# Kernel tuning notes

Hardware: AMD Instinct MI355X
Metric: run time of the kernel (lower is better)

Reference implementation:

```python
import jax, jax.numpy as jnp
import numpy as np

N = 1024      # n_nodes
S = 32        # state_dim
M = 32        # message_dim
STEPS = 5     # n_steps


def setup_inputs() -> dict:
    key = jax.random.key(0)
    ks = jax.random.split(key, 12)
    w = lambda k, shape: jax.random.normal(k, shape, jnp.float32) * 0.02
    return {
        "J": jax.random.normal(ks[0], (N, N), jnp.float32),
        "b": jax.random.normal(ks[1], (N,), jnp.float32),
        # message_passing MLP (Linear(2S+3->M), Linear(M->M), Linear(M->M))
        "W1": w(ks[2], (M, 2 * S + 3)), "b1": jnp.zeros((M,), jnp.float32),
        "W2": w(ks[3], (M, M)),         "b2": jnp.zeros((M,), jnp.float32),
        "W3": w(ks[4], (M, M)),         "b3": jnp.zeros((M,), jnp.float32),
        # GRU(input=S+M, hidden=S). h0 is always zero in the original forward,
        # so weight_hh never contributes (only bias_hh does) and is omitted.
        "W_ih": w(ks[5], (3 * S, S + M)),
        "b_ih": w(ks[6], (3 * S,)),
        "b_hh": w(ks[7], (3 * S,)),
        # readout MLP (Linear(S->M), Linear(M->M), Linear(M->2))
        "R1": w(ks[8], (M, S)),  "rb1": jnp.zeros((M,), jnp.float32),
        "R2": w(ks[9], (M, M)),  "rb2": jnp.zeros((M,), jnp.float32),
        "R3": w(ks[10], (2, M)), "rb3": jnp.zeros((2,), jnp.float32),
    }


def reference(J, b, W1, b1, W2, b2, W3, b3, W_ih, b_ih, b_hh, R1, rb1, R2, rb2, R3, rb3):
    # Split first linear over the concat [h_i, h_j, J_ij, b_i, b_j] so the
    # [N, N, 2S+3] concat tensor is never materialized.
    W1a, W1b = W1[:, :S], W1[:, S:2 * S]
    wJ, wbi, wbj = W1[:, 2 * S], W1[:, 2 * S + 1], W1[:, 2 * S + 2]

    def step(h, _):
        hi = h @ W1a.T                       # [N, M] (sender part)
        hj = h @ W1b.T                       # [N, M] (receiver part)
        pre = (hi[:, None, :] + hj[None, :, :]
               + J[:, :, None] * wJ
               + b[:, None, None] * wbi
               + b[None, :, None] * wbj
               + b1)                          # [N, N, M]
        x = jax.nn.relu(pre)
        x = jax.nn.relu(x @ W2.T + b2)
        x = jax.nn.relu(x @ W3.T + b3)       # message_i_j: [N, N, M]
        m = x.sum(0)                          # message to node j: sum over senders i
        # GRU with zero initial hidden state: h' = (1-z) * n_gate
        gi = jnp.concatenate([h, m], axis=-1) @ W_ih.T + b_ih  # [N, 3S]
        r = jax.nn.sigmoid(gi[:, :S] + b_hh[:S])
        z = jax.nn.sigmoid(gi[:, S:2 * S] + b_hh[S:2 * S])
        n = jnp.tanh(gi[:, 2 * S:] + r * b_hh[2 * S:])
        return (1.0 - z) * n, None

    h0 = jnp.zeros((N, S), J.dtype)
    h, _ = jax.lax.scan(step, h0, None, length=STEPS)

    r = jax.nn.relu(h @ R1.T + rb1)
    r = jax.nn.relu(r @ R2.T + rb2)
    r = jax.nn.relu(r @ R3.T + rb3)          # [N, 2]
    return jax.nn.sigmoid(r)
```

## Files before the change

kernel.cpp:

```cpp
#include <hip/hip_runtime.h>
#include <math.h>

#define NN 1024

typedef __attribute__((ext_vector_type(8))) short bf16x8;
typedef __attribute__((ext_vector_type(4))) float f32x4;
typedef __attribute__((ext_vector_type(4))) unsigned int u32x4;

__device__ __forceinline__ float sigmoidf_(float x) { return 1.0f / (1.0f + __expf(-x)); }

__device__ __forceinline__ unsigned int pk_bf16(float a, float b) {
    unsigned int ua = __float_as_uint(a), ub = __float_as_uint(b);
    ua += 0x7fffu + ((ua >> 16) & 1u);
    ub += 0x7fffu + ((ub >> 16) & 1u);
    return (ua >> 16) | (ub & 0xffff0000u);
}
__device__ __forceinline__ unsigned short f2bf_rne(float a) {
    unsigned int ua = __float_as_uint(a);
    ua += 0x7fffu + ((ua >> 16) & 1u);
    return (unsigned short)(ua >> 16);
}

struct Ctx {
    bf16x8 w2a0, w2a1, w3a0, w3a1;
    f32x4 b2v0, b2v1, b3v0, b3v1;
    float wj8[8];
};

__device__ __forceinline__ void make_ctx(Ctx& c, int p, int q,
    const float* __restrict__ W1, const float* __restrict__ W2,
    const float* __restrict__ b2, const float* __restrict__ W3,
    const float* __restrict__ b3)
{
    union FU { bf16x8 v; unsigned short s[8]; } t0, t1, t2, t3;
#pragma unroll
    for (int jj = 0; jj < 8; jj++) {
        int k = q * 8 + jj;
        t0.s[jj] = f2bf_rne(W2[p * 32 + k]);
        t1.s[jj] = f2bf_rne(W2[(16 + p) * 32 + k]);
        t2.s[jj] = f2bf_rne(W3[p * 32 + k]);
        t3.s[jj] = f2bf_rne(W3[(16 + p) * 32 + k]);
        c.wj8[jj] = W1[k * 67 + 64];
    }
    c.w2a0 = t0.v; c.w2a1 = t1.v; c.w3a0 = t2.v; c.w3a1 = t3.v;
#pragma unroll
    for (int r = 0; r < 4; r++) {
        c.b2v0[r] = b2[q * 4 + r];  c.b2v1[r] = b2[16 + q * 4 + r];
        c.b3v0[r] = b3[q * 4 + r];  c.b3v1[r] = b3[16 + q * 4 + r];
    }
}

__device__ __forceinline__ void gru_row(int s, float hval, float mval, float bj,
    const float* __restrict__ Wih, const float* __restrict__ bih,
    const float* __restrict__ bhh, const float* __restrict__ W1,
    const float* __restrict__ b1, float& hn, float& uacc, float& vacc)
{
    float g0 = bih[s], g1 = bih[32 + s], g2 = bih[64 + s];
#pragma unroll 8
    for (int k = 0; k < 32; k++) {
        float hk = __shfl(hval, k, 32);
        float mk = __shfl(mval, k, 32);
        g0 = fmaf(Wih[s * 64 + k],             hk, g0);
        g0 = fmaf(Wih[s * 64 + 32 + k],        mk, g0);
        g1 = fmaf(Wih[(32 + s) * 64 + k],      hk, g1);
        g1 = fmaf(Wih[(32 + s) * 64 + 32 + k], mk, g1);
        g2 = fmaf(Wih[(64 + s) * 64 + k],      hk, g2);
        g2 = fmaf(Wih[(64 + s) * 64 + 32 + k], mk, g2);
    }
    float r = sigmoidf_(g0 + bhh[s]);
    float z = sigmoidf_(g1 + bhh[32 + s]);
    float n = tanhf(g2 + r * bhh[64 + s]);
    hn = (1.0f - z) * n;
    float ua = bj * W1[s * 67 + 65];
    float va = fmaf(bj, W1[s * 67 + 66], b1[s]);
#pragma unroll 8
    for (int k = 0; k < 32; k++) {
        float hk = __shfl(hn, k, 32);
        ua = fmaf(W1[s * 67 + k],      hk, ua);
        va = fmaf(W1[s * 67 + 32 + k], hk, va);
    }
    uacc = ua; vacc = va;
}

__device__ __forceinline__ void readout_row(int s, int j, float hn,
    const float* __restrict__ R1, const float* __restrict__ rb1,
    const float* __restrict__ R2, const float* __restrict__ rb2,
    const float* __restrict__ R3, const float* __restrict__ rb3,
    float* __restrict__ out)
{
    float a1 = rb1[s];
#pragma unroll 8
    for (int k = 0; k < 32; k++) a1 = fmaf(R1[s * 32 + k], __shfl(hn, k, 32), a1);
    a1 = fmaxf(a1, 0.f);
    float a2 = rb2[s];
#pragma unroll 8
    for (int k = 0; k < 32; k++) a2 = fmaf(R2[s * 32 + k], __shfl(a1, k, 32), a2);
    a2 = fmaxf(a2, 0.f);
    float a3 = (s < 2) ? rb3[s] : 0.f;
#pragma unroll 8
    for (int k = 0; k < 32; k++) {
        float a2k = __shfl(a2, k, 32);
        if (s < 2) a3 = fmaf(R3[s * 32 + k], a2k, a3);
    }
    if (s < 2) out[j * 2 + s] = sigmoidf_(fmaxf(a3, 0.f));
}

__global__ __launch_bounds__(256) void k_pre(
    const float* __restrict__ J, const float* __restrict__ b,
    const float* __restrict__ W1, const float* __restrict__ b1,
    float* __restrict__ Jt, float* __restrict__ h,
    float* __restrict__ u0, float* __restrict__ v)
{
    __shared__ float tile[32][33];
    const int t = blockIdx.x;
    const int tid = threadIdx.x;
    if (t < 1024) {
        int tx = (t & 31) * 32, ty = (t >> 5) * 32;
        int x = tid & 31, y = tid >> 5;
#pragma unroll
        for (int r = 0; r < 4; r++)
            tile[y + 8 * r][x] = J[(size_t)(ty + y + 8 * r) * NN + tx + x];
        __syncthreads();
#pragma unroll
        for (int r = 0; r < 4; r++)
            Jt[(size_t)(tx + y + 8 * r) * NN + ty + x] = tile[x][y + 8 * r];
    } else {
        int idx = (t - 1024) * 256 + tid;
        int row = idx >> 5, mm = idx & 31;
        float bi = b[row];
        h[idx]  = 0.f;
        u0[idx] = bi * W1[mm * 67 + 65];
        v[idx]  = fmaf(bi, W1[mm * 67 + 66], b1[mm]);
    }
}

__global__ __launch_bounds__(256, 4) void k_step(
    const float* __restrict__ Jt, const float* __restrict__ W1,
    const float* __restrict__ W2, const float* __restrict__ b2,
    const float* __restrict__ W3, const float* __restrict__ b3,
    const float* __restrict__ Wih, const float* __restrict__ bih,
    const float* __restrict__ bhh, const float* __restrict__ b,
    const float* __restrict__ b1,
    const float* __restrict__ R1, const float* __restrict__ rb1,
    const float* __restrict__ R2, const float* __restrict__ rb2,
    const float* __restrict__ R3, const float* __restrict__ rb3,
    float* __restrict__ h, float* __restrict__ v,
    const float* __restrict__ ui, float* __restrict__ uo,
    float* __restrict__ out, int do_out)
{
    __shared__ float red[4 * 32];

    const int tid = threadIdx.x;
    const int w = tid >> 6;
    const int l = tid & 63;
    const int p = l & 15;
    const int q = l >> 4;
    const int j = blockIdx.x;

    Ctx c; make_ctx(c, p, q, W1, W2, b2, W3, b3);
    const float* Jtrow = Jt + (size_t)j * NN;

    float vv[8];
#pragma unroll
    for (int jj = 0; jj < 8; jj++) vv[jj] = v[j * 32 + q * 8 + jj];

    const int s0 = (p | ((l & 16) << 1)) << 2;
    const int s1 = s0 + 64;
    const bool qlo = (l & 32) == 0;

    f32x4 acc0 = {0.f, 0.f, 0.f, 0.f}, acc1 = {0.f, 0.f, 0.f, 0.f};

    int i0 = w * 256 + p;
    float  jw = Jtrow[i0];
    float4 ua = *(const float4*)(ui + i0 * 32 + q * 8);
    float4 ub = *(const float4*)(ui + i0 * 32 + q * 8 + 4);

#pragma unroll 2
    for (int t = 0; t < 16; ++t) {
        const float  jw_c = jw;
        const float4 ua_c = ua;
        const float4 ub_c = ub;
        if (t < 15) {
            const int in = w * 256 + (t + 1) * 16 + p;
            jw = Jtrow[in];
            ua = *(const float4*)(ui + in * 32 + q * 8);
            ub = *(const float4*)(ui + in * 32 + q * 8 + 4);
        }

        float xr[8];
        xr[0] = fmaxf(fmaf(jw_c, c.wj8[0], ua_c.x + vv[0]), 0.f);
        xr[1] = fmaxf(fmaf(jw_c, c.wj8[1], ua_c.y + vv[1]), 0.f);
        xr[2] = fmaxf(fmaf(jw_c, c.wj8[2], ua_c.z + vv[2]), 0.f);
        xr[3] = fmaxf(fmaf(jw_c, c.wj8[3], ua_c.w + vv[3]), 0.f);
        xr[4] = fmaxf(fmaf(jw_c, c.wj8[4], ub_c.x + vv[4]), 0.f);
        xr[5] = fmaxf(fmaf(jw_c, c.wj8[5], ub_c.y + vv[5]), 0.f);
        xr[6] = fmaxf(fmaf(jw_c, c.wj8[6], ub_c.z + vv[6]), 0.f);
        xr[7] = fmaxf(fmaf(jw_c, c.wj8[7], ub_c.w + vv[7]), 0.f);

        union BU { u32x4 u4; bf16x8 v; unsigned int d[4]; } bx;
#pragma unroll
        for (int cc = 0; cc < 4; cc++) bx.d[cc] = pk_bf16(xr[2 * cc], xr[2 * cc + 1]);

        f32x4 c0 = __builtin_amdgcn_mfma_f32_16x16x32_bf16(c.w2a0, bx.v, c.b2v0, 0, 0, 0);
        f32x4 c1 = __builtin_amdgcn_mfma_f32_16x16x32_bf16(c.w2a1, bx.v, c.b2v1, 0, 0, 0);

        const int d0 = (int)pk_bf16(fmaxf(c0[0], 0.f), fmaxf(c0[1], 0.f));
        const int d1 = (int)pk_bf16(fmaxf(c0[2], 0.f), fmaxf(c0[3], 0.f));
        const int d2 = (int)pk_bf16(fmaxf(c1[0], 0.f), fmaxf(c1[1], 0.f));
        const int d3 = (int)pk_bf16(fmaxf(c1[2], 0.f), fmaxf(c1[3], 0.f));

        const int A0 = __builtin_amdgcn_ds_bpermute(s0, d0);
        const int A1 = __builtin_amdgcn_ds_bpermute(s0, d1);
        const int A2 = __builtin_amdgcn_ds_bpermute(s1, d0);
        const int A3 = __builtin_amdgcn_ds_bpermute(s1, d1);
        const int B0 = __builtin_amdgcn_ds_bpermute(s0, d2);
        const int B1 = __builtin_amdgcn_ds_bpermute(s0, d3);
        const int B2 = __builtin_amdgcn_ds_bpermute(s1, d2);
        const int B3 = __builtin_amdgcn_ds_bpermute(s1, d3);

        union BU yr;
        yr.d[0] = (unsigned)(qlo ? A0 : B0);
        yr.d[1] = (unsigned)(qlo ? A1 : B1);
        yr.d[2] = (unsigned)(qlo ? A2 : B2);
        yr.d[3] = (unsigned)(qlo ? A3 : B3);

        f32x4 e0 = __builtin_amdgcn_mfma_f32_16x16x32_bf16(c.w3a0, yr.v, c.b3v0, 0, 0, 0);
        f32x4 e1 = __builtin_amdgcn_mfma_f32_16x16x32_bf16(c.w3a1, yr.v, c.b3v1, 0, 0, 0);
#pragma unroll
        for (int r = 0; r < 4; r++) {
            acc0[r] += fmaxf(e0[r], 0.f);
            acc1[r] += fmaxf(e1[r], 0.f);
        }
    }

#pragma unroll
    for (int bit = 1; bit < 16; bit <<= 1) {
#pragma unroll
        for (int r = 0; r < 4; r++) {
            acc0[r] += __shfl_xor(acc0[r], bit);
            acc1[r] += __shfl_xor(acc1[r], bit);
        }
    }
    if (p == 0) {
#pragma unroll
        for (int r = 0; r < 4; r++) {
            red[w * 32 + q * 4 + r]      = acc0[r];
            red[w * 32 + 16 + q * 4 + r] = acc1[r];
        }
    }
    __syncthreads();

    if (tid < 32) {
        const int s = tid;
        float mval = red[s] + red[32 + s] + red[64 + s] + red[96 + s];
        float hn, uacc, vacc;
        gru_row(s, h[j * 32 + s], mval, b[j], Wih, bih, bhh, W1, b1, hn, uacc, vacc);
        h[j * 32 + s] = hn;
        v[j * 32 + s] = vacc;
        uo[j * 32 + s] = uacc;
        if (do_out) readout_row(s, j, hn, R1, rb1, R2, rb2, R3, rb3, out);
    }
}

extern "C" void kernel_launch(void* const* d_in, const int* in_sizes, int n_in,
                              void* d_out, int out_size, void* d_ws, size_t ws_size,
                              hipStream_t stream)
{
    const float* J   = (const float*)d_in[0];
    const float* b   = (const float*)d_in[1];
    const float* W1  = (const float*)d_in[2];
    const float* b1  = (const float*)d_in[3];
    const float* W2  = (const float*)d_in[4];
    const float* b2  = (const float*)d_in[5];
    const float* W3  = (const float*)d_in[6];
    const float* b3  = (const float*)d_in[7];
    const float* Wih = (const float*)d_in[8];
    const float* bih = (const float*)d_in[9];
    const float* bhh = (const float*)d_in[10];
    const float* R1  = (const float*)d_in[11];
    const float* rb1 = (const float*)d_in[12];
    const float* R2  = (const float*)d_in[13];
    const float* rb2 = (const float*)d_in[14];
    const float* R3  = (const float*)d_in[15];
    const float* rb3 = (const float*)d_in[16];

    float* out = (float*)d_out;
    float* ws  = (float*)d_ws;
    float* h  = ws;
    float* v  = ws + 32768;
    float* u0 = ws + 65536;
    float* u1 = ws + 98304;
    float* Jt = ws + 131072;

    k_pre<<<1152, 256, 0, stream>>>(J, b, W1, b1, Jt, h, u0, v);
    for (int s = 0; s < 5; s++) {
        const float* ui = (s & 1) ? u1 : u0;
        float*       uo = (s & 1) ? u0 : u1;
        k_step<<<1024, 256, 0, stream>>>(Jt, W1, W2, b2, W3, b3, Wih, bih,
                                         bhh, b, b1, R1, rb1, R2, rb2, R3,
                                         rb3, h, v, ui, uo, out,
                                         (s == 4) ? 1 : 0);
    }
}
```

Measured before the change: 223.2 us.

## Parallelize GRU and readout tail across threads and deepen operand prefetch

Replaces the 32-lane shuffle-based GRU, message-projection and readout with shared-memory staged dot products spread over up to 192 threads using vectorized weight loads. The main loop now prefetches two iterations ahead with alternating register sets. The first step launches a doubled grid whose extra blocks redo the message loop and then exit. This adds wasted work and extra barriers in exchange for a shorter serial tail.

Measured after the change: 241.4 us. +8.1%, slower.

```diff
diff --git a/kernel.cpp b/kernel.cpp
--- a/kernel.cpp
+++ b/kernel.cpp
@@ -48,61 +48,6 @@
         c.b2v0[r] = b2[q * 4 + r];  c.b2v1[r] = b2[16 + q * 4 + r];
         c.b3v0[r] = b3[q * 4 + r];  c.b3v1[r] = b3[16 + q * 4 + r];
     }
-}
-
-__device__ __forceinline__ void gru_row(int s, float hval, float mval, float bj,
-    const float* __restrict__ Wih, const float* __restrict__ bih,
-    const float* __restrict__ bhh, const float* __restrict__ W1,
-    const float* __restrict__ b1, float& hn, float& uacc, float& vacc)
-{
-    float g0 = bih[s], g1 = bih[32 + s], g2 = bih[64 + s];
-#pragma unroll 8
-    for (int k = 0; k < 32; k++) {
-        float hk = __shfl(hval, k, 32);
-        float mk = __shfl(mval, k, 32);
-        g0 = fmaf(Wih[s * 64 + k],             hk, g0);
-        g0 = fmaf(Wih[s * 64 + 32 + k],        mk, g0);
-        g1 = fmaf(Wih[(32 + s) * 64 + k],      hk, g1);
-        g1 = fmaf(Wih[(32 + s) * 64 + 32 + k], mk, g1);
-        g2 = fmaf(Wih[(64 + s) * 64 + k],      hk, g2);
-        g2 = fmaf(Wih[(64 + s) * 64 + 32 + k], mk, g2);
-    }
-    float r = sigmoidf_(g0 + bhh[s]);
-    float z = sigmoidf_(g1 + bhh[32 + s]);
-    float n = tanhf(g2 + r * bhh[64 + s]);
-    hn = (1.0f - z) * n;
-    float ua = bj * W1[s * 67 + 65];
-    float va = fmaf(bj, W1[s * 67 + 66], b1[s]);
-#pragma unroll 8
-    for (int k = 0; k < 32; k++) {
-        float hk = __shfl(hn, k, 32);
-        ua = fmaf(W1[s * 67 + k],      hk, ua);
-        va = fmaf(W1[s * 67 + 32 + k], hk, va);
-    }
-    uacc = ua; vacc = va;
-}
-
-__device__ __forceinline__ void readout_row(int s, int j, float hn,
-    const float* __restrict__ R1, const float* __restrict__ rb1,
-    const float* __restrict__ R2, const float* __restrict__ rb2,
-    const float* __restrict__ R3, const float* __restrict__ rb3,
-    float* __restrict__ out)
-{
-    float a1 = rb1[s];
-#pragma unroll 8
-    for (int k = 0; k < 32; k++) a1 = fmaf(R1[s * 32 + k], __shfl(hn, k, 32), a1);
-    a1 = fmaxf(a1, 0.f);
-    float a2 = rb2[s];
-#pragma unroll 8
-    for (int k = 0; k < 32; k++) a2 = fmaf(R2[s * 32 + k], __shfl(a1, k, 32), a2);
-    a2 = fmaxf(a2, 0.f);
-    float a3 = (s < 2) ? rb3[s] : 0.f;
-#pragma unroll 8
-    for (int k = 0; k < 32; k++) {
-        float a2k = __shfl(a2, k, 32);
-        if (s < 2) a3 = fmaf(R3[s * 32 + k], a2k, a3);
-    }
-    if (s < 2) out[j * 2 + s] = sigmoidf_(fmaxf(a3, 0.f));
 }
 
 __global__ __launch_bounds__(256) void k_pre(
@@ -149,13 +94,18 @@
     float* __restrict__ out, int do_out)
 {
     __shared__ float red[4 * 32];
+    __shared__ float hm[64];
+    __shared__ float gbuf[96];
+    __shared__ float hnb[32];
+    __shared__ float tb[32];
 
     const int tid = threadIdx.x;
     const int w = tid >> 6;
     const int l = tid & 63;
     const int p = l & 15;
     const int q = l >> 4;
-    const int j = blockIdx.x;
+    const int j = blockIdx.x & 1023;
+    const bool primary = (blockIdx.x < 1024);
 
     Ctx c; make_ctx(c, p, q, W1, W2, b2, W3, b3);
     const float* Jtrow = Jt + (size_t)j * NN;
@@ -170,21 +120,31 @@
 
     f32x4 acc0 = {0.f, 0.f, 0.f, 0.f}, acc1 = {0.f, 0.f, 0.f, 0.f};
 
-    int i0 = w * 256 + p;
-    float  jw = Jtrow[i0];
-    float4 ua = *(const float4*)(ui + i0 * 32 + q * 8);
-    float4 ub = *(const float4*)(ui + i0 * 32 + q * 8 + 4);
-
-#pragma unroll 2
+    const int ibase = w * 256;
+    float  jwA = Jtrow[ibase + p];
+    float4 uaA = *(const float4*)(ui + (ibase + p) * 32 + q * 8);
+    float4 ubA = *(const float4*)(ui + (ibase + p) * 32 + q * 8 + 4);
+    float  jwB = Jtrow[ibase + 16 + p];
+    float4 uaB = *(const float4*)(ui + (ibase + 16 + p) * 32 + q * 8);
+    float4 ubB = *(const float4*)(ui + (ibase + 16 + p) * 32 + q * 8 + 4);
+
+#pragma unroll 4
     for (int t = 0; t < 16; ++t) {
-        const float  jw_c = jw;
-        const float4 ua_c = ua;
-        const float4 ub_c = ub;
-        if (t < 15) {
-            const int in = w * 256 + (t + 1) * 16 + p;
-            jw = Jtrow[in];
-            ua = *(const float4*)(ui + in * 32 + q * 8);
-            ub = *(const float4*)(ui + in * 32 + q * 8 + 4);
+        float  jw_c;
+        float4 ua_c, ub_c;
+        if ((t & 1) == 0) { jw_c = jwA; ua_c = uaA; ub_c = ubA; }
+        else              { jw_c = jwB; ua_c = uaB; ub_c = ubB; }
+        if (t < 14) {
+            const int in = ibase + (t + 2) * 16 + p;
+            if ((t & 1) == 0) {
+                jwA = Jtrow[in];
+                uaA = *(const float4*)(ui + in * 32 + q * 8);
+                ubA = *(const float4*)(ui + in * 32 + q * 8 + 4);
+            } else {
+                jwB = Jtrow[in];
+                uaB = *(const float4*)(ui + in * 32 + q * 8);
+                ubB = *(const float4*)(ui + in * 32 + q * 8 + 4);
+            }
         }
 
         float xr[8];
@@ -248,17 +208,99 @@
             red[w * 32 + 16 + q * 4 + r] = acc1[r];
         }
     }
+
+    if (!primary) return;
+    __syncthreads();
+
+    if (tid < 64) {
+        float val;
+        if (tid < 32) val = h[j * 32 + tid];
+        else {
+            int s = tid - 32;
+            val = red[s] + red[32 + s] + red[64 + s] + red[96 + s];
+        }
+        hm[tid] = val;
+    }
+    __syncthreads();
+
+    if (tid < 192) {
+        const int row = tid >> 1, half = tid & 1;
+        const float* wr = Wih + row * 64 + half * 32;
+        const float* hh = hm + half * 32;
+        float acc = 0.f;
+#pragma unroll
+        for (int k4 = 0; k4 < 8; k4++) {
+            float4 w4 = *(const float4*)(wr + 4 * k4);
+            acc = fmaf(w4.x, hh[4 * k4 + 0], acc);
+            acc = fmaf(w4.y, hh[4 * k4 + 1], acc);
+            acc = fmaf(w4.z, hh[4 * k4 + 2], acc);
+            acc = fmaf(w4.w, hh[4 * k4 + 3], acc);
+        }
+        acc += __shfl_xor(acc, 1);
+        if (half == 0) gbuf[row] = acc + bih[row];
+    }
     __syncthreads();
 
     if (tid < 32) {
         const int s = tid;
-        float mval = red[s] + red[32 + s] + red[64 + s] + red[96 + s];
-        float hn, uacc, vacc;
-        gru_row(s, h[j * 32 + s], mval, b[j], Wih, bih, bhh, W1, b1, hn, uacc, vacc);
-        h[j * 32 + s] = hn;
-        v[j * 32 + s] = vacc;
-        uo[j * 32 + s] = uacc;
-        if (do_out) readout_row(s, j, hn, R1, rb1, R2, rb2, R3, rb3, out);
+        float r = sigmoidf_(gbuf[s] + bhh[s]);
+        float z = sigmoidf_(gbuf[32 + s] + bhh[32 + s]);
+        float n = tanhf(gbuf[64 + s] + r * bhh[64 + s]);
+        float hn_ = (1.0f - z) * n;
+        hnb[s] = hn_;
+        h[j * 32 + s] = hn_;
+    }
+    __syncthreads();
+
+    if (tid < 64) {
+        const int s = tid & 31;
+        const bool isV = tid >= 32;
+        const float bj = b[j];
+        const float* wr = W1 + s * 67 + (isV ? 32 : 0);
+        float acc = isV ? fmaf(bj, W1[s * 67 + 66], b1[s]) : bj * W1[s * 67 + 65];
+#pragma unroll
+        for (int k = 0; k < 32; k++) acc = fmaf(wr[k], hnb[k], acc);
+        if (isV) v[j * 32 + s] = acc;
+        else     uo[j * 32 + s] = acc;
+    }
+
+    if (do_out) {
+        __syncthreads();
+        if (tid < 32) {
+            float a = rb1[tid];
+            const float* rr = R1 + tid * 32;
+#pragma unroll
+            for (int k4 = 0; k4 < 8; k4++) {
+                float4 w4 = *(const float4*)(rr + 4 * k4);
+                a = fmaf(w4.x, hnb[4 * k4 + 0], a);
+                a = fmaf(w4.y, hnb[4 * k4 + 1], a);
+                a = fmaf(w4.z, hnb[4 * k4 + 2], a);
+                a = fmaf(w4.w, hnb[4 * k4 + 3], a);
+            }
+            gbuf[tid] = fmaxf(a, 0.f);
+        }
+        __syncthreads();
+        if (tid < 32) {
+            float a = rb2[tid];
+            const float* rr = R2 + tid * 32;
+#pragma unroll
+            for (int k4 = 0; k4 < 8; k4++) {
+                float4 w4 = *(const float4*)(rr + 4 * k4);
+                a = fmaf(w4.x, gbuf[4 * k4 + 0], a);
+                a = fmaf(w4.y, gbuf[4 * k4 + 1], a);
+                a = fmaf(w4.z, gbuf[4 * k4 + 2], a);
+                a = fmaf(w4.w, gbuf[4 * k4 + 3], a);
+            }
+            tb[tid] = fmaxf(a, 0.f);
+        }
+        __syncthreads();
+        if (tid < 2) {
+            float a = rb3[tid];
+            const float* rr = R3 + tid * 32;
+#pragma unroll
+            for (int k = 0; k < 32; k++) a = fmaf(rr[k], tb[k], a);
+            out[j * 2 + tid] = sigmoidf_(fmaxf(a, 0.f));
+        }
     }
 }
 
@@ -296,7 +338,8 @@
     for (int s = 0; s < 5; s++) {
         const float* ui = (s & 1) ? u1 : u0;
         float*       uo = (s & 1) ? u0 : u1;
-        k_step<<<1024, 256, 0, stream>>>(Jt, W1, W2, b2, W3, b3, Wih, bih,
+        int grid = (s == 0) ? 2048 : 1024;
+        k_step<<<grid, 256, 0, stream>>>(Jt, W1, W2, b2, W3, b3, Wih, bih,
                                          bhh, b, b1, R1, rb1, R2, rb2, R3,
                                          rb3, h, v, ui, uo, out,
                                          (s == 4) ? 1 : 0);
```
